# Kernel optimization log

Hardware: AMD Instinct MI355X
Metric: run time of the kernel (lower is better)

Reference implementation:

```python
import jax, jax.numpy as jnp
import numpy as np

N_NODES = 100000
N_EDGES = 1600000
D_FEAT = 128
N_CLASSES = 2
K_HOPS = 2


def setup_inputs() -> dict:
    key = jax.random.key(0)
    k1, k2, k3, k4 = jax.random.split(key, 4)
    x = jax.random.normal(k1, (N_NODES, D_FEAT), dtype=jnp.float32)
    edge_index = jax.random.randint(k2, (2, N_EDGES), 0, N_NODES, dtype=jnp.int64)
    weight = jax.random.normal(k3, (N_CLASSES, D_FEAT), dtype=jnp.float32) * (1.0 / np.sqrt(D_FEAT))
    bias = jnp.zeros((N_CLASSES,), dtype=jnp.float32)
    return {"x": x, "edge_index": edge_index, "weight": weight, "bias": bias}


def reference(x, edge_index, weight, bias):
    N = x.shape[0]
    # gcn_norm with self-loops (PyG SGConv default)
    loop = jnp.arange(N, dtype=edge_index.dtype)
    row = jnp.concatenate([edge_index[0], loop])  # source nodes
    col = jnp.concatenate([edge_index[1], loop])  # target nodes
    ones = jnp.ones(row.shape[0], dtype=x.dtype)
    deg = jax.ops.segment_sum(ones, col, num_segments=N)
    dinv = jnp.where(deg > 0, jax.lax.rsqrt(deg), 0.0)
    norm = dinv[row] * dinv[col]  # [E+N]

    # K hops of normalized sparse propagation: x <- A_norm @ x
    for _ in range(K_HOPS):
        x = jax.ops.segment_sum(x[row] * norm[:, None], col, num_segments=N)

    logits = x @ weight.T + bias  # [N, num_classes]
    return jax.nn.log_softmax(logits, axis=1)
```

## Files before the change

kernel.cpp:

```cpp
#include <hip/hip_runtime.h>

#define D_FEAT 128
#define BSH    8
#define BNODES 256
#define MAXNB  400
#define NSEG   512
#define SEGCAP 16
#define SENT   0xFFFFFFFFu
#define OVPB   32
#define MVB    2048
#define HTB    1024

typedef unsigned u32x4 __attribute__((ext_vector_type(4)));

__global__ __launch_bounds__(256) void k_fused(const float* __restrict__ x,
                                               const int* __restrict__ row,
                                               const int* __restrict__ col,
                                               const float* __restrict__ w,
                                               unsigned long long* __restrict__ ovbuf,
                                               unsigned* __restrict__ ovcnt,
                                               unsigned* __restrict__ gbuf,
                                               float2* __restrict__ zvec,
                                               int E, int n, int NB) {
    __shared__ unsigned lcnt[MAXNB];
    __shared__ unsigned lbuf[MAXNB * SEGCAP];
    __shared__ unsigned lov;
    const int blk = blockIdx.x, tid = threadIdx.x;

    if (blk < NSEG) {
        for (int i = tid; i < NB; i += 256) lcnt[i] = 0;
        if (tid == 0) lov = 0;
        __syncthreads();

        const int chunk = (E + NSEG - 1) / NSEG;
        const int s = blk * chunk;
        const int e_end = min(s + chunk, E);
        for (int e = s + tid; e < e_end; e += 256) {
            int r = row[e], c = col[e];
            int b = c >> BSH;
            unsigned pos = atomicAdd(&lcnt[b], 1u);
            if (pos < SEGCAP) {
                lbuf[b * SEGCAP + pos] = ((unsigned)r << BSH) | (unsigned)(c & (BNODES - 1));
            } else {
                unsigned gi = atomicAdd(&lov, 1u);
                if (gi < OVPB)
                    ovbuf[(size_t)blk * OVPB + gi] =
                        ((unsigned long long)(unsigned)r << 32) | (unsigned)c;
            }
        }
        __syncthreads();

        if (tid == 0) {
            unsigned used = lov; if (used > OVPB) used = OVPB;
            ovcnt[blk] = used;
        }

        const int total4 = NB * (SEGCAP / 4);
        uint4* g4 = (uint4*)gbuf;
        for (int idx = tid; idx < total4; idx += 256) {
            int b = idx >> 2, sg = (idx & 3) * 4;
            unsigned c2 = lcnt[b]; if (c2 > SEGCAP) c2 = SEGCAP;
            const unsigned* lb = &lbuf[b * SEGCAP + sg];
            uint4 v;
            v.x = ((unsigned)(sg + 0) < c2) ? lb[0] : SENT;
            v.y = ((unsigned)(sg + 1) < c2) ? lb[1] : SENT;
            v.z = ((unsigned)(sg + 2) < c2) ? lb[2] : SENT;
            v.w = ((unsigned)(sg + 3) < c2) ? lb[3] : SENT;
            g4[(((size_t)b * NSEG + blk) * SEGCAP + sg) >> 2] = v;
        }
    } else {
        const int lane = tid & 63;
        const float2 w0 = *(const float2*)(w + 2 * lane);
        const float2 w1 = *(const float2*)(w + D_FEAT + 2 * lane);
        const int wave0 = ((blk - NSEG) * 256 + tid) >> 6;
        const int nwaves = (MVB * 256) >> 6;
        for (int node = wave0; node < n; node += nwaves) {
            const float2 xv = *(const float2*)(x + (size_t)node * D_FEAT + 2 * lane);
            float p0 = xv.x * w0.x + xv.y * w0.y;
            float p1 = xv.x * w1.x + xv.y * w1.y;
            #pragma unroll
            for (int off = 32; off > 0; off >>= 1) {
                p0 += __shfl_down(p0, off, 64);
                p1 += __shfl_down(p1, off, 64);
            }
            if (lane == 0) zvec[node] = make_float2(p0, p1);
        }
    }
}

__global__ __launch_bounds__(HTB) void k_degnode(const unsigned* __restrict__ gbuf,
                                                 const unsigned long long* __restrict__ ovbuf,
                                                 const unsigned* __restrict__ ovcnt,
                                                 const float2* __restrict__ z,
                                                 float* __restrict__ dinv,
                                                 float2* __restrict__ zd, int n) {
    __shared__ unsigned hist[BNODES];
    __shared__ unsigned ocnt[NSEG];
    const int b = blockIdx.x, tid = threadIdx.x;
    if (tid < BNODES) hist[tid] = 0u;
    for (int i = tid; i < NSEG; i += HTB) ocnt[i] = ovcnt[i];
    __syncthreads();

    const u32x4* p4 = (const u32x4*)(gbuf + (size_t)b * NSEG * SEGCAP);
    const int NIT = (NSEG * SEGCAP / 4) / HTB;
    #pragma unroll
    for (int k = 0; k < NIT; ++k) {
        u32x4 v = p4[tid + k * HTB];
        #pragma unroll
        for (int q = 0; q < 4; ++q)
            if (v[q] != SENT) atomicAdd(&hist[v[q] & (BNODES - 1)], 1u);
    }
    for (int t = tid; t < NSEG; t += HTB) {
        unsigned cntt = ocnt[t];
        for (unsigned i = 0; i < cntt; ++i) {
            unsigned long long e = ovbuf[(size_t)t * OVPB + i];
            unsigned c = (unsigned)e;
            if ((int)(c >> BSH) == b) atomicAdd(&hist[c & (BNODES - 1)], 1u);
        }
    }
    __syncthreads();

    if (tid < BNODES) {
        int c = (b << BSH) + tid;
        if (c < n) {
            float d = rsqrtf((float)hist[tid] + 1.0f);
            dinv[c] = d;
            float2 zi = z[c];
            zd[c] = make_float2(zi.x * d, zi.y * d);
        }
    }
}

__global__ __launch_bounds__(HTB) void k_hop(const unsigned* __restrict__ gbuf,
                                             const unsigned long long* __restrict__ ovbuf,
                                             const unsigned* __restrict__ ovcnt,
                                             const float2* __restrict__ vin,
                                             const float* __restrict__ dinv,
                                             const float* __restrict__ bias,
                                             float2* __restrict__ outv,
                                             int n, int mode) {
    __shared__ float accx[BNODES];
    __shared__ float accy[BNODES];
    __shared__ unsigned ocnt[NSEG];
    const int b = blockIdx.x, tid = threadIdx.x;
    if (tid < BNODES) { accx[tid] = 0.f; accy[tid] = 0.f; }
    for (int i = tid; i < NSEG; i += HTB) ocnt[i] = ovcnt[i];
    __syncthreads();

    const u32x4* p4 = (const u32x4*)(gbuf + (size_t)b * NSEG * SEGCAP);
    const int NIT = (NSEG * SEGCAP / 4) / HTB;
    #pragma unroll
    for (int k = 0; k < NIT; ++k) {
        u32x4 v = p4[tid + k * HTB];
        #pragma unroll
        for (int q = 0; q < 4; ++q) {
            unsigned ent = v[q];
            if (ent != SENT) {
                float2 s = vin[ent >> BSH];
                atomicAdd(&accx[ent & (BNODES - 1)], s.x);
                atomicAdd(&accy[ent & (BNODES - 1)], s.y);
            }
        }
    }
    for (int t = tid; t < NSEG; t += HTB) {
        unsigned cntt = ocnt[t];
        for (unsigned i = 0; i < cntt; ++i) {
            unsigned long long e = ovbuf[(size_t)t * OVPB + i];
            unsigned c = (unsigned)e;
            if ((int)(c >> BSH) == b) {
                float2 s = vin[e >> 32];
                atomicAdd(&accx[c & (BNODES - 1)], s.x);
                atomicAdd(&accy[c & (BNODES - 1)], s.y);
            }
        }
    }
    __syncthreads();

    if (tid < BNODES) {
        int c = (b << BSH) + tid;
        if (c < n) {
            float d = dinv[c];
            float2 s = vin[c];
            float ax = s.x + accx[tid];
            float ay = s.y + accy[tid];
            if (mode == 0) {
                float dd = d * d;
                outv[c] = make_float2(ax * dd, ay * dd);
            } else {
                float l0 = ax * d + bias[0];
                float l1 = ay * d + bias[1];
                float mx = fmaxf(l0, l1);
                float lse = mx + logf(expf(l0 - mx) + expf(l1 - mx));
                outv[c] = make_float2(l0 - lse, l1 - lse);
            }
        }
    }
}


__global__ __launch_bounds__(256) void k_matvec(const float* __restrict__ x,
                                                const float* __restrict__ w,
                                                float2* __restrict__ z, int n) {
    int wave = (int)((blockIdx.x * blockDim.x + threadIdx.x) >> 6);
    int lane = threadIdx.x & 63;
    if (wave >= n) return;
    const float2 xv = *(const float2*)(x + (size_t)wave * D_FEAT + 2 * lane);
    const float2 w0 = *(const float2*)(w + 2 * lane);
    const float2 w1 = *(const float2*)(w + D_FEAT + 2 * lane);
    float p0 = xv.x * w0.x + xv.y * w0.y;
    float p1 = xv.x * w1.x + xv.y * w1.y;
    #pragma unroll
    for (int off = 32; off > 0; off >>= 1) {
        p0 += __shfl_down(p0, off, 64);
        p1 += __shfl_down(p1, off, 64);
    }
    if (lane == 0) z[wave] = make_float2(p0, p1);
}

__global__ __launch_bounds__(256) void k_deg(const int* __restrict__ col,
                                             unsigned int* __restrict__ deg, int E) {
    int e = blockIdx.x * blockDim.x + threadIdx.x;
    if (e < E) atomicAdd(&deg[col[e]], 1u);
}

__global__ __launch_bounds__(256) void k_dinv_init(const unsigned int* __restrict__ deg,
                                                   float* __restrict__ dinv,
                                                   const float2* __restrict__ zin,
                                                   float2* __restrict__ yout, int n) {
    int i = blockIdx.x * blockDim.x + threadIdx.x;
    if (i < n) {
        float d = rsqrtf((float)deg[i] + 1.0f);
        dinv[i] = d;
        float2 zi = zin[i];
        float dd = d * d;
        yout[i] = make_float2(zi.x * dd, zi.y * dd);
    }
}

__global__ __launch_bounds__(256) void k_selfloop(const float* __restrict__ dinv,
                                                  const float2* __restrict__ zin,
                                                  float2* __restrict__ yout, int n) {
    int i = blockIdx.x * blockDim.x + threadIdx.x;
    if (i < n) {
        float d = dinv[i];
        float dd = d * d;
        float2 zi = zin[i];
        yout[i] = make_float2(zi.x * dd, zi.y * dd);
    }
}

__global__ __launch_bounds__(256) void k_edge(const int* __restrict__ row,
                                              const int* __restrict__ col,
                                              const float* __restrict__ dinv,
                                              const float2* __restrict__ zin,
                                              float* __restrict__ yout, int E) {
    int e = blockIdx.x * blockDim.x + threadIdx.x;
    if (e < E) {
        int r = row[e], c = col[e];
        float nr = dinv[r] * dinv[c];
        float2 zr = zin[r];
        atomicAdd(&yout[2 * c + 0], zr.x * nr);
        atomicAdd(&yout[2 * c + 1], zr.y * nr);
    }
}

__global__ __launch_bounds__(256) void k_final(const float2* __restrict__ y,
                                               const float* __restrict__ bias,
                                               float2* __restrict__ out, int n) {
    int i = blockIdx.x * blockDim.x + threadIdx.x;
    if (i < n) {
        float2 l = y[i];
        float l0 = l.x + bias[0];
        float l1 = l.y + bias[1];
        float m = fmaxf(l0, l1);
        float lse = m + logf(expf(l0 - m) + expf(l1 - m));
        out[i] = make_float2(l0 - lse, l1 - lse);
    }
}

extern "C" void kernel_launch(void* const* d_in, const int* in_sizes, int n_in,
                              void* d_out, int out_size, void* d_ws, size_t ws_size,
                              hipStream_t stream) {
    const float* x    = (const float*)d_in[0];
    const int*   ei   = (const int*)d_in[1];
    const float* w    = (const float*)d_in[2];
    const float* bias = (const float*)d_in[3];

    const int n = in_sizes[0] / D_FEAT;
    const int E = in_sizes[1] / 2;
    const int* row = ei;
    const int* col = ei + E;

    const int TB = 256;
    const int nodeBlocks = (n + TB - 1) / TB;
    const int edgeBlocks = (E + TB - 1) / TB;
    const int waveBlocks = (n + 3) / 4;

    const int NB = (n + BNODES - 1) >> BSH;

    size_t need = (size_t)NSEG * OVPB * 8
                + (size_t)NSEG * 4
                + (size_t)NB * NSEG * SEGCAP * 4
                + (size_t)n * 8 * 3
                + (size_t)n * 4;

    if (NB <= MAXNB && n < (1 << 24) && ws_size >= need) {
        char* ws = (char*)d_ws;
        unsigned long long* ovbuf = (unsigned long long*)ws; ws += (size_t)NSEG * OVPB * 8;
        unsigned* ovcnt = (unsigned*)ws;                     ws += (size_t)NSEG * 4;
        unsigned* gbuf = (unsigned*)ws;                      ws += (size_t)NB * NSEG * SEGCAP * 4;
        float2* zvec   = (float2*)ws;                        ws += (size_t)n * 8;
        float2* zd     = (float2*)ws;                        ws += (size_t)n * 8;
        float2* y1d    = (float2*)ws;                        ws += (size_t)n * 8;
        float*  dinv   = (float*)ws;

        k_fused  <<<NSEG + MVB, TB, 0, stream>>>(x, row, col, w, ovbuf, ovcnt,
                                                 gbuf, zvec, E, n, NB);
        k_degnode<<<NB, HTB, 0, stream>>>(gbuf, ovbuf, ovcnt, zvec, dinv, zd, n);
        k_hop    <<<NB, HTB, 0, stream>>>(gbuf, ovbuf, ovcnt, zd, dinv, bias,
                                          y1d, n, 0);
        k_hop    <<<NB, HTB, 0, stream>>>(gbuf, ovbuf, ovcnt, y1d, dinv, bias,
                                          (float2*)d_out, n, 1);
    } else {
        char* ws = (char*)d_ws;
        float2* z   = (float2*)ws; ws += (size_t)n * sizeof(float2);
        float2* y1  = (float2*)ws; ws += (size_t)n * sizeof(float2);
        float2* y2  = (float2*)ws; ws += (size_t)n * sizeof(float2);
        float*  dinv = (float*)ws; ws += (size_t)n * sizeof(float);
        unsigned int* deg = (unsigned int*)ws;

        (void)hipMemsetAsync(deg, 0, (size_t)n * sizeof(unsigned int), stream);
        k_deg<<<edgeBlocks, TB, 0, stream>>>(col, deg, E);
        k_matvec<<<waveBlocks, TB, 0, stream>>>(x, w, z, n);
        k_dinv_init<<<nodeBlocks, TB, 0, stream>>>(deg, dinv, z, y1, n);
        k_edge<<<edgeBlocks, TB, 0, stream>>>(row, col, dinv, z, (float*)y1, E);
        k_selfloop<<<nodeBlocks, TB, 0, stream>>>(dinv, y1, y2, n);
        k_edge<<<edgeBlocks, TB, 0, stream>>>(row, col, dinv, y1, (float*)y2, E);
        k_final<<<nodeBlocks, TB, 0, stream>>>(y2, bias, (float2*)d_out, n);
    }
}
```

Before: 165.6 us.

## Fuse degree and both hops into one cooperative kernel with grid syncs

Merges the degree/normalization kernel and the two propagation hops into a single cooperative kernel, using grid.sync between phases. Per-block dinv and self-loop values stay in shared memory, so the global dinv buffer and its reloads go away. This removes two kernel launches and their tail gaps. The cost is two grid-wide barriers and the requirement that all NB blocks (about 391 blocks of 1024 threads) be co-resident for the cooperative launch to succeed.

```diff
diff --git a/kernel.cpp b/kernel.cpp
--- a/kernel.cpp
+++ b/kernel.cpp
@@ -1,4 +1,7 @@
 #include <hip/hip_runtime.h>
+#include <hip/hip_cooperative_groups.h>
+
+namespace cg = cooperative_groups;
 
 #define D_FEAT 128
 #define BSH    8
@@ -88,21 +91,31 @@
     }
 }
 
-__global__ __launch_bounds__(HTB) void k_degnode(const unsigned* __restrict__ gbuf,
+__global__ __launch_bounds__(HTB, 8) void k_coop(const unsigned* __restrict__ gbuf,
                                                  const unsigned long long* __restrict__ ovbuf,
                                                  const unsigned* __restrict__ ovcnt,
-                                                 const float2* __restrict__ z,
-                                                 float* __restrict__ dinv,
-                                                 float2* __restrict__ zd, int n) {
+                                                 const float2* __restrict__ zvec,
+                                                 float2* __restrict__ zd,
+                                                 float2* __restrict__ y1d,
+                                                 const float* __restrict__ bias,
+                                                 float2* __restrict__ out, int n) {
     __shared__ unsigned hist[BNODES];
+    __shared__ float accx[BNODES];
+    __shared__ float accy[BNODES];
     __shared__ unsigned ocnt[NSEG];
+    __shared__ float ldinv[BNODES];
+    __shared__ float2 lself[BNODES];
+
+    cg::grid_group grid = cg::this_grid();
     const int b = blockIdx.x, tid = threadIdx.x;
+    const int c = (b << BSH) + tid;
+    const u32x4* p4 = (const u32x4*)(gbuf + (size_t)b * NSEG * SEGCAP);
+    const int NIT = (NSEG * SEGCAP / 4) / HTB;
+
     if (tid < BNODES) hist[tid] = 0u;
     for (int i = tid; i < NSEG; i += HTB) ocnt[i] = ovcnt[i];
     __syncthreads();
 
-    const u32x4* p4 = (const u32x4*)(gbuf + (size_t)b * NSEG * SEGCAP);
-    const int NIT = (NSEG * SEGCAP / 4) / HTB;
     #pragma unroll
     for (int k = 0; k < NIT; ++k) {
         u32x4 v = p4[tid + k * HTB];
@@ -114,41 +127,26 @@
         unsigned cntt = ocnt[t];
         for (unsigned i = 0; i < cntt; ++i) {
             unsigned long long e = ovbuf[(size_t)t * OVPB + i];
-            unsigned c = (unsigned)e;
-            if ((int)(c >> BSH) == b) atomicAdd(&hist[c & (BNODES - 1)], 1u);
-        }
-    }
-    __syncthreads();
-
-    if (tid < BNODES) {
-        int c = (b << BSH) + tid;
-        if (c < n) {
-            float d = rsqrtf((float)hist[tid] + 1.0f);
-            dinv[c] = d;
-            float2 zi = z[c];
-            zd[c] = make_float2(zi.x * d, zi.y * d);
-        }
-    }
-}
-
-__global__ __launch_bounds__(HTB) void k_hop(const unsigned* __restrict__ gbuf,
-                                             const unsigned long long* __restrict__ ovbuf,
-                                             const unsigned* __restrict__ ovcnt,
-                                             const float2* __restrict__ vin,
-                                             const float* __restrict__ dinv,
-                                             const float* __restrict__ bias,
-                                             float2* __restrict__ outv,
-                                             int n, int mode) {
-    __shared__ float accx[BNODES];
-    __shared__ float accy[BNODES];
-    __shared__ unsigned ocnt[NSEG];
-    const int b = blockIdx.x, tid = threadIdx.x;
+            unsigned cc = (unsigned)e;
+            if ((int)(cc >> BSH) == b) atomicAdd(&hist[cc & (BNODES - 1)], 1u);
+        }
+    }
+    __syncthreads();
+
+    if (tid < BNODES && c < n) {
+        float d = rsqrtf((float)hist[tid] + 1.0f);
+        ldinv[tid] = d;
+        float2 zi = zvec[c];
+        float2 s = make_float2(zi.x * d, zi.y * d);
+        lself[tid] = s;
+        zd[c] = s;
+    }
+    __threadfence();
+    grid.sync();
+
     if (tid < BNODES) { accx[tid] = 0.f; accy[tid] = 0.f; }
-    for (int i = tid; i < NSEG; i += HTB) ocnt[i] = ovcnt[i];
-    __syncthreads();
-
-    const u32x4* p4 = (const u32x4*)(gbuf + (size_t)b * NSEG * SEGCAP);
-    const int NIT = (NSEG * SEGCAP / 4) / HTB;
+    __syncthreads();
+
     #pragma unroll
     for (int k = 0; k < NIT; ++k) {
         u32x4 v = p4[tid + k * HTB];
@@ -156,7 +154,7 @@
         for (int q = 0; q < 4; ++q) {
             unsigned ent = v[q];
             if (ent != SENT) {
-                float2 s = vin[ent >> BSH];
+                float2 s = zd[ent >> BSH];
                 atomicAdd(&accx[ent & (BNODES - 1)], s.x);
                 atomicAdd(&accy[ent & (BNODES - 1)], s.y);
             }
@@ -166,34 +164,64 @@
         unsigned cntt = ocnt[t];
         for (unsigned i = 0; i < cntt; ++i) {
             unsigned long long e = ovbuf[(size_t)t * OVPB + i];
-            unsigned c = (unsigned)e;
-            if ((int)(c >> BSH) == b) {
-                float2 s = vin[e >> 32];
-                atomicAdd(&accx[c & (BNODES - 1)], s.x);
-                atomicAdd(&accy[c & (BNODES - 1)], s.y);
-            }
-        }
-    }
-    __syncthreads();
-
-    if (tid < BNODES) {
-        int c = (b << BSH) + tid;
-        if (c < n) {
-            float d = dinv[c];
-            float2 s = vin[c];
-            float ax = s.x + accx[tid];
-            float ay = s.y + accy[tid];
-            if (mode == 0) {
-                float dd = d * d;
-                outv[c] = make_float2(ax * dd, ay * dd);
-            } else {
-                float l0 = ax * d + bias[0];
-                float l1 = ay * d + bias[1];
-                float mx = fmaxf(l0, l1);
-                float lse = mx + logf(expf(l0 - mx) + expf(l1 - mx));
-                outv[c] = make_float2(l0 - lse, l1 - lse);
-            }
-        }
+            unsigned cc = (unsigned)e;
+            if ((int)(cc >> BSH) == b) {
+                float2 s = zd[e >> 32];
+                atomicAdd(&accx[cc & (BNODES - 1)], s.x);
+                atomicAdd(&accy[cc & (BNODES - 1)], s.y);
+            }
+        }
+    }
+    __syncthreads();
+
+    if (tid < BNODES && c < n) {
+        float d = ldinv[tid], dd = d * d;
+        float2 s = lself[tid];
+        float2 y = make_float2((s.x + accx[tid]) * dd, (s.y + accy[tid]) * dd);
+        lself[tid] = y;
+        y1d[c] = y;
+    }
+    __threadfence();
+    grid.sync();
+
+    if (tid < BNODES) { accx[tid] = 0.f; accy[tid] = 0.f; }
+    __syncthreads();
+
+    #pragma unroll
+    for (int k = 0; k < NIT; ++k) {
+        u32x4 v = p4[tid + k * HTB];
+        #pragma unroll
+        for (int q = 0; q < 4; ++q) {
+            unsigned ent = v[q];
+            if (ent != SENT) {
+                float2 s = y1d[ent >> BSH];
+                atomicAdd(&accx[ent & (BNODES - 1)], s.x);
+                atomicAdd(&accy[ent & (BNODES - 1)], s.y);
+            }
+        }
+    }
+    for (int t = tid; t < NSEG; t += HTB) {
+        unsigned cntt = ocnt[t];
+        for (unsigned i = 0; i < cntt; ++i) {
+            unsigned long long e = ovbuf[(size_t)t * OVPB + i];
+            unsigned cc = (unsigned)e;
+            if ((int)(cc >> BSH) == b) {
+                float2 s = y1d[e >> 32];
+                atomicAdd(&accx[cc & (BNODES - 1)], s.x);
+                atomicAdd(&accy[cc & (BNODES - 1)], s.y);
+            }
+        }
+    }
+    __syncthreads();
+
+    if (tid < BNODES && c < n) {
+        float d = ldinv[tid];
+        float2 s = lself[tid];
+        float l0 = (s.x + accx[tid]) * d + bias[0];
+        float l1 = (s.y + accy[tid]) * d + bias[1];
+        float mx = fmaxf(l0, l1);
+        float lse = mx + logf(expf(l0 - mx) + expf(l1 - mx));
+        out[c] = make_float2(l0 - lse, l1 - lse);
     }
 }
 
@@ -301,8 +329,7 @@
     size_t need = (size_t)NSEG * OVPB * 8
                 + (size_t)NSEG * 4
                 + (size_t)NB * NSEG * SEGCAP * 4
-                + (size_t)n * 8 * 3
-                + (size_t)n * 4;
+                + (size_t)n * 8 * 3;
 
     if (NB <= MAXNB && n < (1 << 24) && ws_size >= need) {
         char* ws = (char*)d_ws;
@@ -311,16 +338,19 @@
         unsigned* gbuf = (unsigned*)ws;                      ws += (size_t)NB * NSEG * SEGCAP * 4;
         float2* zvec   = (float2*)ws;                        ws += (size_t)n * 8;
         float2* zd     = (float2*)ws;                        ws += (size_t)n * 8;
-        float2* y1d    = (float2*)ws;                        ws += (size_t)n * 8;
-        float*  dinv   = (float*)ws;
-
-        k_fused  <<<NSEG + MVB, TB, 0, stream>>>(x, row, col, w, ovbuf, ovcnt,
-                                                 gbuf, zvec, E, n, NB);
-        k_degnode<<<NB, HTB, 0, stream>>>(gbuf, ovbuf, ovcnt, zvec, dinv, zd, n);
-        k_hop    <<<NB, HTB, 0, stream>>>(gbuf, ovbuf, ovcnt, zd, dinv, bias,
-                                          y1d, n, 0);
-        k_hop    <<<NB, HTB, 0, stream>>>(gbuf, ovbuf, ovcnt, y1d, dinv, bias,
-                                          (float2*)d_out, n, 1);
+        float2* y1d    = (float2*)ws;
+
+        k_fused<<<NSEG + MVB, TB, 0, stream>>>(x, row, col, w, ovbuf, ovcnt,
+                                               gbuf, zvec, E, n, NB);
+
+        float2* outp = (float2*)d_out;
+        int nn = n;
+        void* args[] = {
+            (void*)&gbuf, (void*)&ovbuf, (void*)&ovcnt, (void*)&zvec,
+            (void*)&zd, (void*)&y1d, (void*)&bias, (void*)&outp, (void*)&nn
+        };
+        (void)hipLaunchCooperativeKernel((void*)k_coop, dim3(NB), dim3(HTB),
+                                         args, 0, stream);
     } else {
         char* ws = (char*)d_ws;
         float2* z   = (float2*)ws; ws += (size_t)n * sizeof(float2);
```

Result: slower. 428.3 us (+158.6%).
